# Kernel tuning notes

Measured on AMD Instinct MI355X. Metric: run time of the kernel, lower is better.

## Reference

```python
import jax, jax.numpy as jnp
import numpy as np

HIDDEN = 2048
N_HEADS = 32
N_KV_HEADS = 8
HEAD_DIM = HIDDEN // N_HEADS  # 64
N_GROUPS = N_HEADS // N_KV_HEADS  # 4
EPS = 1e-6
BATCH = 2
SEQ = 2048


def setup_inputs() -> dict:
    key = jax.random.key(0)
    ks = jax.random.split(key, 8)
    s = 1.0 / np.sqrt(HIDDEN)
    return {
        "hidden_states": jax.random.normal(ks[0], (BATCH, SEQ, HIDDEN), jnp.float32),
        # torch nn.Linear weights: [out_features, in_features]
        "Wq": jax.random.normal(ks[1], (N_HEADS * HEAD_DIM, HIDDEN), jnp.float32) * s,
        "Wk": jax.random.normal(ks[2], (N_KV_HEADS * HEAD_DIM, HIDDEN), jnp.float32) * s,
        "Wv": jax.random.normal(ks[3], (N_KV_HEADS * HEAD_DIM, HIDDEN), jnp.float32) * s,
        "Wo": jax.random.normal(ks[4], (HIDDEN, N_HEADS * HEAD_DIM), jnp.float32) * s,
        "q_norm_weight": jnp.ones((HEAD_DIM,), jnp.float32),
        "k_norm_weight": jnp.ones((HEAD_DIM,), jnp.float32),
    }


def _rmsnorm(x, w, eps=EPS):
    # x: [..., head_dim]
    rms = jax.lax.rsqrt(jnp.mean(x * x, axis=-1, keepdims=True) + eps)
    return x * rms * w


def reference(hidden_states, Wq, Wk, Wv, Wo, q_norm_weight, k_norm_weight):
    B, S, _ = hidden_states.shape
    # projections (y = x @ W.T)
    q = jnp.einsum('bsh,oh->bso', hidden_states, Wq)
    k = jnp.einsum('bsh,oh->bso', hidden_states, Wk)
    v = jnp.einsum('bsh,oh->bso', hidden_states, Wv)
    # [B, H, S, D]
    q = q.reshape(B, S, N_HEADS, HEAD_DIM).transpose(0, 2, 1, 3)
    k = k.reshape(B, S, N_KV_HEADS, HEAD_DIM).transpose(0, 2, 1, 3)
    v = v.reshape(B, S, N_KV_HEADS, HEAD_DIM).transpose(0, 2, 1, 3)
    # GQA repeat_interleave along head dim
    k = jnp.repeat(k, N_GROUPS, axis=1)
    v = jnp.repeat(v, N_GROUPS, axis=1)
    # fused QK RMSNorm
    q = _rmsnorm(q, q_norm_weight)
    k = _rmsnorm(k, k_norm_weight)
    # scaled dot-product attention with causal mask
    scale = 1.0 / np.sqrt(HEAD_DIM)
    scores = jnp.einsum('bhqd,bhkd->bhqk', q, k) * scale
    causal = jnp.tril(jnp.ones((S, S), dtype=bool))
    scores = jnp.where(causal, scores, jnp.finfo(scores.dtype).min)
    attn = jax.nn.softmax(scores, axis=-1)
    out = jnp.einsum('bhqk,bhkd->bhqd', attn, v)  # [B, H, S, D]
    out = out.transpose(0, 2, 1, 3).reshape(B, S, N_HEADS * HEAD_DIM)
    return jnp.einsum('bso,ho->bsh', out, Wo)
```

## Files before the change

### kernel.cpp

```cpp
#include <hip/hip_runtime.h>

typedef _Float16 f16;
typedef _Float16 f16x8 __attribute__((ext_vector_type(8)));
typedef _Float16 f16x4 __attribute__((ext_vector_type(4)));
typedef __fp16 fp16x2 __attribute__((ext_vector_type(2)));
typedef float f32x4 __attribute__((ext_vector_type(4)));

#define HID 2048
#define NH 32
#define NKV 8
#define HD 64
#define SEQ 2048
#define NB 2

__device__ __forceinline__ void gload_lds16(const void* g, void* l) {
  __builtin_amdgcn_global_load_lds((const __attribute__((address_space(1))) void*)g,
                                   (__attribute__((address_space(3))) void*)l, 16, 0, 0);
}

__device__ __forceinline__ uint cvt_pk_f16(float a, float b) {
  auto v = __builtin_amdgcn_cvt_pkrtz(a, b);
  uint u;
  __builtin_memcpy(&u, &v, 4);
  return u;
}

__device__ __forceinline__ float fdot2_ones(uint pk, float acc) {
  fp16x2 a;
  __builtin_memcpy(&a, &pk, 4);
  fp16x2 ones = {(__fp16)1.0f, (__fp16)1.0f};
  return __builtin_amdgcn_fdot2(a, ones, acc, false);
}

__device__ __forceinline__ float fast_exp2(float x) {
  float r;
  asm("v_exp_f32 %0, %1" : "=v"(r) : "v"(x));
  return r;
}

__global__ __launch_bounds__(256) void cvt_all(const float* __restrict__ X,
                                               const float* __restrict__ Wq,
                                               const float* __restrict__ Wk,
                                               const float* __restrict__ Wv,
                                               const float* __restrict__ Wo,
                                               f16* __restrict__ Xb, f16* __restrict__ Wqb,
                                               f16* __restrict__ Wkb, f16* __restrict__ Wvb,
                                               f16* __restrict__ Wob) {
  long i = (long)blockIdx.x * 256 + threadIdx.x;
  const float* s; f16* d; long o;
  if (i < 2097152)      { s = X;  d = Xb;  o = i; }
  else if (i < 3145728) { s = Wq; d = Wqb; o = i - 2097152; }
  else if (i < 3407872) { s = Wk; d = Wkb; o = i - 3145728; }
  else if (i < 3670016) { s = Wv; d = Wvb; o = i - 3407872; }
  else                  { s = Wo; d = Wob; o = i - 3670016; }
  float4 v = ((const float4*)s)[o];
  f16x4 ov = { (f16)v.x, (f16)v.y, (f16)v.z, (f16)v.w };
  ((f16x4*)d)[o] = ov;
}

__global__ __launch_bounds__(512, 2) void gemm256(const f16* __restrict__ A,
                                                  const f16* __restrict__ Bm,
                                                  f16* __restrict__ C0, f16* __restrict__ C1,
                                                  int M, int N, int K,
                                                  int n_split, int ldc0, int ldc1) {
  __shared__ f16 As[2][256 * 64];
  __shared__ f16 Bs[2][256 * 64];
  const int t = threadIdx.x, lane = t & 63, w = t >> 6;
  const int wr = w >> 2, wc = w & 3;
  const int g = lane >> 4, lr = lane & 15;

  const int nwg = gridDim.x * gridDim.y;
  const int orig = blockIdx.y * gridDim.x + blockIdx.x;
  const int wg = (orig & 7) * (nwg >> 3) + (orig >> 3);
  const int m0 = (wg / gridDim.x) * 256;
  const int n0 = (wg % gridDim.x) * 256;

  f32x4 acc[8][4] = {};
  const int nkt = K / 64;

  auto stage = [&](int buf, int kt) {
    const int k0 = kt * 64;
#pragma unroll
    for (int i = 0; i < 4; ++i) {
      int c = w * 4 + i;
      int o = c * 1024 + lane * 16;
      int row = o >> 7;
      int ss = ((o >> 4) & 7) ^ (row & 7);
      gload_lds16((const char*)A + ((size_t)(m0 + row) * K + k0) * 2 + ss * 16,
                  (char*)(&As[buf][0]) + c * 1024);
      gload_lds16((const char*)Bm + ((size_t)(n0 + row) * K + k0) * 2 + ss * 16,
                  (char*)(&Bs[buf][0]) + c * 1024);
    }
  };

  stage(0, 0);
  stage(1, 1);
  for (int kt = 0; kt < nkt; ++kt) {
    const int cur = kt & 1;
    if (kt + 1 < nkt) asm volatile("s_waitcnt vmcnt(8)" ::: "memory");
    else              asm volatile("s_waitcnt vmcnt(0)" ::: "memory");
    __builtin_amdgcn_s_barrier();
    __builtin_amdgcn_sched_barrier(0);

    const char* Ab = (const char*)(&As[cur][0]);
    const char* Bb = (const char*)(&Bs[cur][0]);
    f16x8 af[2][4], bf[2][4];

#pragma unroll
    for (int ks = 0; ks < 2; ++ks)
#pragma unroll
      for (int mf = 0; mf < 4; ++mf) {
        int row = wr * 128 + mf * 16 + lr;
        af[ks][mf] = *(const f16x8*)(Ab + row * 128 + (((g + 4 * ks) ^ (row & 7)) * 16));
      }
#pragma unroll
    for (int ks = 0; ks < 2; ++ks)
#pragma unroll
      for (int nf = 0; nf < 2; ++nf) {
        int row = wc * 64 + nf * 16 + lr;
        bf[ks][nf] = *(const f16x8*)(Bb + row * 128 + (((g + 4 * ks) ^ (row & 7)) * 16));
      }
    __builtin_amdgcn_s_setprio(1);
#pragma unroll
    for (int ks = 0; ks < 2; ++ks)
#pragma unroll
      for (int mf = 0; mf < 4; ++mf)
#pragma unroll
        for (int nf = 0; nf < 2; ++nf)
          acc[mf][nf] = __builtin_amdgcn_mfma_f32_16x16x32_f16(af[ks][mf], bf[ks][nf], acc[mf][nf], 0, 0, 0);
    __builtin_amdgcn_s_setprio(0);
    __builtin_amdgcn_sched_barrier(0);

#pragma unroll
    for (int ks = 0; ks < 2; ++ks)
#pragma unroll
      for (int nf = 2; nf < 4; ++nf) {
        int row = wc * 64 + nf * 16 + lr;
        bf[ks][nf] = *(const f16x8*)(Bb + row * 128 + (((g + 4 * ks) ^ (row & 7)) * 16));
      }
    __builtin_amdgcn_s_setprio(1);
#pragma unroll
    for (int ks = 0; ks < 2; ++ks)
#pragma unroll
      for (int mf = 0; mf < 4; ++mf)
#pragma unroll
        for (int nf = 2; nf < 4; ++nf)
          acc[mf][nf] = __builtin_amdgcn_mfma_f32_16x16x32_f16(af[ks][mf], bf[ks][nf], acc[mf][nf], 0, 0, 0);
    __builtin_amdgcn_s_setprio(0);
    __builtin_amdgcn_sched_barrier(0);

#pragma unroll
    for (int ks = 0; ks < 2; ++ks)
#pragma unroll
      for (int mf = 0; mf < 4; ++mf) {
        int row = wr * 128 + (mf + 4) * 16 + lr;
        af[ks][mf] = *(const f16x8*)(Ab + row * 128 + (((g + 4 * ks) ^ (row & 7)) * 16));
      }
    __builtin_amdgcn_s_setprio(1);
#pragma unroll
    for (int ks = 0; ks < 2; ++ks)
#pragma unroll
      for (int mf = 0; mf < 4; ++mf)
#pragma unroll
        for (int nf = 0; nf < 2; ++nf)
          acc[mf + 4][nf] = __builtin_amdgcn_mfma_f32_16x16x32_f16(af[ks][mf], bf[ks][nf], acc[mf + 4][nf], 0, 0, 0);
    __builtin_amdgcn_s_setprio(0);
    __builtin_amdgcn_sched_barrier(0);

    __builtin_amdgcn_s_setprio(1);
#pragma unroll
    for (int ks = 0; ks < 2; ++ks)
#pragma unroll
      for (int mf = 0; mf < 4; ++mf)
#pragma unroll
        for (int nf = 2; nf < 4; ++nf)
          acc[mf + 4][nf] = __builtin_amdgcn_mfma_f32_16x16x32_f16(af[ks][mf], bf[ks][nf], acc[mf + 4][nf], 0, 0, 0);
    __builtin_amdgcn_s_setprio(0);
    __builtin_amdgcn_sched_barrier(0);

    __builtin_amdgcn_s_barrier();
    __builtin_amdgcn_sched_barrier(0);
    if (kt + 2 < nkt) stage(cur, kt + 2);
  }

  f16* Cp; int ldc, nb;
  if (n0 < n_split) { Cp = C0; ldc = ldc0; nb = n0; }
  else              { Cp = C1; ldc = ldc1; nb = n0 - n_split; }
#pragma unroll
  for (int mf = 0; mf < 8; ++mf)
#pragma unroll
    for (int nf = 0; nf < 4; ++nf)
#pragma unroll
      for (int r = 0; r < 4; ++r) {
        int mm = m0 + wr * 128 + mf * 16 + g * 4 + r;
        int nn = nb + wc * 64 + nf * 16 + lr;
        Cp[(size_t)mm * ldc + nn] = (f16)acc[mf][nf][r];
      }
}

template <typename CT>
__global__ __launch_bounds__(256) void gemm_bt(const f16* __restrict__ A,
                                               const f16* __restrict__ Bm,
                                               CT* __restrict__ C0, CT* __restrict__ C1,
                                               int M, int N, int K,
                                               int n_split, int ldc0, int ldc1) {
  __shared__ f16 As[2][128 * 64];
  __shared__ f16 Bs[2][128 * 64];
  const int t = threadIdx.x;
  const int lane = t & 63;
  const int w = t >> 6;
  const int wr = w >> 1, wc = w & 1;
  const int g = lane >> 4;
  const int lr = lane & 15;

  const int nwg = gridDim.x * gridDim.y;
  const int orig = blockIdx.y * gridDim.x + blockIdx.x;
  const int wg = (orig & 7) * (nwg >> 3) + (orig >> 3);
  const int m0 = (wg / gridDim.x) * 128;
  const int n0 = (wg % gridDim.x) * 128;

  f32x4 acc[4][4] = {};

  const int nkt = K / 64;

  auto stage = [&](int buf, int kt) {
    const int k0 = kt * 64;
#pragma unroll
    for (int i = 0; i < 4; ++i) {
      int c = w * 4 + i;
      int o = c * 1024 + lane * 16;
      int row = o >> 7;
      int ss = ((o >> 4) & 7) ^ (row & 7);
      const char* srcA = (const char*)A + ((size_t)(m0 + row) * K + k0) * 2 + ss * 16;
      gload_lds16(srcA, (char*)(&As[buf][0]) + c * 1024);
      const char* srcB = (const char*)Bm + ((size_t)(n0 + row) * K + k0) * 2 + ss * 16;
      gload_lds16(srcB, (char*)(&Bs[buf][0]) + c * 1024);
    }
  };

  stage(0, 0);
  if (nkt > 1) stage(1, 1);
  for (int kt = 0; kt < nkt; ++kt) {
    const int cur = kt & 1;
    if (kt + 1 < nkt) asm volatile("s_waitcnt vmcnt(8)" ::: "memory");
    else              asm volatile("s_waitcnt vmcnt(0)" ::: "memory");
    __builtin_amdgcn_s_barrier();
    __builtin_amdgcn_sched_barrier(0);

    f16x8 af[2][4], bf[2][4];
#pragma unroll
    for (int ks = 0; ks < 2; ++ks)
#pragma unroll
      for (int mf = 0; mf < 4; ++mf) {
        int row = wr * 64 + mf * 16 + lr;
        int slot = (g + 4 * ks) ^ (row & 7);
        af[ks][mf] = *(const f16x8*)((const char*)(&As[cur][0]) + row * 128 + slot * 16);
      }
#pragma unroll
    for (int ks = 0; ks < 2; ++ks)
#pragma unroll
      for (int nf = 0; nf < 4; ++nf) {
        int row = wc * 64 + nf * 16 + lr;
        int slot = (g + 4 * ks) ^ (row & 7);
        bf[ks][nf] = *(const f16x8*)((const char*)(&Bs[cur][0]) + row * 128 + slot * 16);
      }
    asm volatile("s_waitcnt lgkmcnt(0)" ::: "memory");
    __builtin_amdgcn_sched_barrier(0);
    __builtin_amdgcn_s_barrier();

    if (kt + 2 < nkt) stage(cur, kt + 2);

    __builtin_amdgcn_s_setprio(1);
#pragma unroll
    for (int ks = 0; ks < 2; ++ks)
#pragma unroll
      for (int mf = 0; mf < 4; ++mf)
#pragma unroll
        for (int nf = 0; nf < 4; ++nf)
          acc[mf][nf] = __builtin_amdgcn_mfma_f32_16x16x32_f16(af[ks][mf], bf[ks][nf], acc[mf][nf], 0, 0, 0);
    __builtin_amdgcn_s_setprio(0);
  }

  CT* Cp; int ldc, nb;
  if (n0 < n_split) { Cp = C0; ldc = ldc0; nb = n0; }
  else              { Cp = C1; ldc = ldc1; nb = n0 - n_split; }
#pragma unroll
  for (int mf = 0; mf < 4; ++mf)
#pragma unroll
    for (int nf = 0; nf < 4; ++nf)
#pragma unroll
      for (int r = 0; r < 4; ++r) {
        int mm = m0 + wr * 64 + mf * 16 + g * 4 + r;
        int nn = nb + wc * 64 + nf * 16 + lr;
        Cp[(size_t)mm * ldc + nn] = (CT)acc[mf][nf][r];
      }
}

__global__ __launch_bounds__(256) void vtrans(f16* __restrict__ KV,
                                              f16* __restrict__ VT,
                                              const float* __restrict__ kw) {
  __shared__ f16 tile[64][72];
  int t = threadIdx.x;
  int st = blockIdx.x, hk = blockIdx.y, b = blockIdx.z;

#pragma unroll
  for (int p = 0; p < 2; ++p) {
    int idx = p * 256 + t;
    int s = idx >> 3, c8 = (idx & 7) * 8;
    f16* kp = KV + (size_t)(b * SEQ + st * 64 + s) * 1024 + hk * 64 + c8;
    f16x8 kv = *(const f16x8*)kp;
    float ss = 0.f;
#pragma unroll
    for (int j = 0; j < 8; ++j) { float x = (float)kv[j]; ss += x * x; }
    ss += __shfl_xor(ss, 1); ss += __shfl_xor(ss, 2); ss += __shfl_xor(ss, 4);
    float sc = rsqrtf(ss * (1.0f / 64.0f) + 1e-6f);
    f16x8 on;
#pragma unroll
    for (int j = 0; j < 8; ++j) on[j] = (f16)((float)kv[j] * sc * kw[c8 + j]);
    *(f16x8*)kp = on;
  }

#pragma unroll
  for (int p = 0; p < 2; ++p) {
    int idx = p * 256 + t;
    int s = idx >> 3, c8 = (idx & 7) * 8;
    f16x8 v = *(const f16x8*)(KV + (size_t)(b * SEQ + st * 64 + s) * 1024 + 512 + hk * 64 + c8);
    *(f16x8*)(&tile[s][c8]) = v;
  }
  __syncthreads();
#pragma unroll
  for (int p = 0; p < 2; ++p) {
    int idx = p * 256 + t;
    int d = idx >> 3, s8 = (idx & 7) * 8;
    f16x8 ov;
#pragma unroll
    for (int j = 0; j < 8; ++j) {
      int pos = s8 + j;
      int k = (pos & 32) | (((pos >> 2) & 1) << 4) | (((pos >> 4) & 1) << 3)
            | (((pos >> 3) & 1) << 2) | (pos & 3);
      ov[j] = tile[k][d];
    }
    *(f16x8*)(VT + ((size_t)((b * NKV + hk) * 64) + d) * SEQ + st * 64 + s8) = ov;
  }
}

__global__ __launch_bounds__(512) void attn(const f16* __restrict__ Q,
                                            const f16* __restrict__ KV,
                                            const f16* __restrict__ VT,
                                            f16* __restrict__ AO,
                                            const float* __restrict__ qw) {
  __shared__ f16 Ks[3][64 * 64];
  __shared__ f16 Vs[3][64 * 64];
  const int t = threadIdx.x, lane = t & 63, w = t >> 6;
  const int g = lane >> 4, lr = lane & 15;
  const int col = blockIdx.x;
  const int qt = 31 - blockIdx.y;
  const int b = col & 1;
  const int h = 2 * (col >> 1) + (w >> 2);
  const int rg = w & 3;
  const int hk = h >> 2;
  const int q0 = qt * 64;

  const size_t qrow = (size_t)(b * SEQ + q0 + rg * 16 + lr);
  f16x8 qf[2];
  qf[0] = *(const f16x8*)(Q + qrow * HID + h * 64 + g * 8);
  qf[1] = *(const f16x8*)(Q + qrow * HID + h * 64 + g * 8 + 32);

  {
    float ss = 0.f;
#pragma unroll
    for (int i = 0; i < 2; ++i)
#pragma unroll
      for (int j = 0; j < 8; ++j) { float x = (float)qf[i][j]; ss += x * x; }
    ss += __shfl_xor(ss, 16); ss += __shfl_xor(ss, 32);
    float sc = rsqrtf(ss * (1.0f / 64.0f) + 1e-6f) * (0.125f * 1.44269504f);
    const float4* qw4 = (const float4*)qw;
    float4 w0 = qw4[2 * g], w1 = qw4[2 * g + 1];
    float4 w2 = qw4[2 * g + 8], w3 = qw4[2 * g + 9];
    qf[0][0] = (f16)((float)qf[0][0] * sc * w0.x);
    qf[0][1] = (f16)((float)qf[0][1] * sc * w0.y);
    qf[0][2] = (f16)((float)qf[0][2] * sc * w0.z);
    qf[0][3] = (f16)((float)qf[0][3] * sc * w0.w);
    qf[0][4] = (f16)((float)qf[0][4] * sc * w1.x);
    qf[0][5] = (f16)((float)qf[0][5] * sc * w1.y);
    qf[0][6] = (f16)((float)qf[0][6] * sc * w1.z);
    qf[0][7] = (f16)((float)qf[0][7] * sc * w1.w);
    qf[1][0] = (f16)((float)qf[1][0] * sc * w2.x);
    qf[1][1] = (f16)((float)qf[1][1] * sc * w2.y);
    qf[1][2] = (f16)((float)qf[1][2] * sc * w2.z);
    qf[1][3] = (f16)((float)qf[1][3] * sc * w2.w);
    qf[1][4] = (f16)((float)qf[1][4] * sc * w3.x);
    qf[1][5] = (f16)((float)qf[1][5] * sc * w3.y);
    qf[1][6] = (f16)((float)qf[1][6] * sc * w3.z);
    qf[1][7] = (f16)((float)qf[1][7] * sc * w3.w);
  }

  int koff[2][4], voff[2][4];
#pragma unroll
  for (int ks = 0; ks < 2; ++ks)
#pragma unroll
    for (int nf = 0; nf < 4; ++nf) {
      int row = nf * 16 + lr;
      koff[ks][nf] = row * 128 + (((g + 4 * ks) ^ (row & 7)) * 16);
    }
#pragma unroll
  for (int m = 0; m < 2; ++m)
#pragma unroll
    for (int df = 0; df < 4; ++df) {
      int row = df * 16 + lr;
      voff[m][df] = row * 128 + (((4 * m + g) ^ (row & 7)) * 16);
    }

  f32x4 oacc[4] = {};
  float psum0 = 0.0f, psum1 = 0.0f;

  const int nkt = qt + 1;

  auto stage = [&](int buf, int kt2) {
    int o = w * 1024 + lane * 16;
    int row = o >> 7;
    int ss = ((o >> 4) & 7) ^ (row & 7);
    gload_lds16((const char*)KV + ((size_t)(b * SEQ + kt2 * 64 + row) * 1024 + hk * 64) * 2 + ss * 16,
                (char*)(&Ks[buf][0]) + w * 1024);
    gload_lds16((const char*)VT + (((size_t)((b * NKV + hk) * 64) + row) * SEQ + kt2 * 64) * 2 + ss * 16,
                (char*)(&Vs[buf][0]) + w * 1024);
  };

  stage(0, 0);
  if (nkt > 1) stage(1, 1);
  int cur = 0;
  for (int kt = 0; kt < nkt; ++kt) {
    if (kt + 1 < nkt) asm volatile("s_waitcnt vmcnt(2)" ::: "memory");
    else              asm volatile("s_waitcnt vmcnt(0)" ::: "memory");
    __builtin_amdgcn_s_barrier();
    asm volatile("" ::: "memory");

    if (kt + 2 < nkt) {
      int nb = cur + 2; if (nb >= 3) nb -= 3;
      stage(nb, kt + 2);
    }

    const char* Kb = (const char*)(&Ks[cur][0]);
    const char* Vb = (const char*)(&Vs[cur][0]);

    f32x4 sacc[4] = {};
#pragma unroll
    for (int ks = 0; ks < 2; ++ks) {
      __builtin_amdgcn_s_setprio(1);
#pragma unroll
      for (int nf = 0; nf < 4; ++nf) {
        f16x8 kf = *(const f16x8*)(Kb + koff[ks][nf]);
        sacc[nf] = __builtin_amdgcn_mfma_f32_16x16x32_f16(kf, qf[ks], sacc[nf], 0, 0, 0);
      }
      __builtin_amdgcn_s_setprio(0);
    }

    if (kt == qt) {
      int qq = q0 + rg * 16 + lr;
#pragma unroll
      for (int nf = 0; nf < 4; ++nf) {
        int kvb = kt * 64 + nf * 16 + g * 4;
#pragma unroll
        for (int r = 0; r < 4; ++r)
          if (kvb + r > qq) sacc[nf][r] = -1e30f;
      }
    }

    uint pk[8];
#pragma unroll
    for (int nf = 0; nf < 4; ++nf) {
      float p0 = fast_exp2(sacc[nf][0]);
      float p1 = fast_exp2(sacc[nf][1]);
      float p2 = fast_exp2(sacc[nf][2]);
      float p3 = fast_exp2(sacc[nf][3]);
      pk[2 * nf]     = cvt_pk_f16(p0, p1);
      pk[2 * nf + 1] = cvt_pk_f16(p2, p3);
      psum0 = fdot2_ones(pk[2 * nf], psum0);
      psum1 = fdot2_ones(pk[2 * nf + 1], psum1);
    }

#pragma unroll
    for (int m = 0; m < 2; ++m) {
      union { uint u[4]; f16x8 v; } pu;
      pu.u[0] = pk[4 * m];     pu.u[1] = pk[4 * m + 1];
      pu.u[2] = pk[4 * m + 2]; pu.u[3] = pk[4 * m + 3];
      __builtin_amdgcn_s_setprio(1);
#pragma unroll
      for (int df = 0; df < 4; ++df) {
        f16x8 vf = *(const f16x8*)(Vb + voff[m][df]);
        oacc[df] = __builtin_amdgcn_mfma_f32_16x16x32_f16(pu.v, vf, oacc[df], 0, 0, 0);
      }
      __builtin_amdgcn_s_setprio(0);
    }

    cur = (cur == 2) ? 0 : cur + 1;
  }

  float psum = psum0 + psum1;
  psum += __shfl_xor(psum, 16);
  psum += __shfl_xor(psum, 32);
  float pdiv[4];
#pragma unroll
  for (int r = 0; r < 4; ++r) pdiv[r] = 1.0f / __shfl(psum, g * 4 + r);

#pragma unroll
  for (int df = 0; df < 4; ++df)
#pragma unroll
    for (int r = 0; r < 4; ++r) {
      size_t rowg = (size_t)(b * SEQ + q0 + rg * 16 + g * 4 + r);
      AO[rowg * HID + h * 64 + df * 16 + lr] = (f16)(oacc[df][r] * pdiv[r]);
    }
}

extern "C" void kernel_launch(void* const* d_in, const int* in_sizes, int n_in,
                              void* d_out, int out_size, void* d_ws, size_t ws_size,
                              hipStream_t stream) {
  const float* X  = (const float*)d_in[0];
  const float* Wq = (const float*)d_in[1];
  const float* Wk = (const float*)d_in[2];
  const float* Wv = (const float*)d_in[3];
  const float* Wo = (const float*)d_in[4];
  const float* qw = (const float*)d_in[5];
  const float* kw = (const float*)d_in[6];

  char* ws = (char*)d_ws;
  f16* Xb   = (f16*)(ws + 0);
  f16* Wqkv = (f16*)(ws + 16777216);
  f16* Wob  = (f16*)(ws + 29360128);
  f16* Qb   = (f16*)(ws + 37748736);
  f16* KVb  = (f16*)(ws + 54525952);
  f16* VTb  = (f16*)(ws + 62914560);
  f16* AOb  = (f16*)(ws + 67108864);
  float* OUT = (float*)d_out;

  cvt_all<<<18432, 256, 0, stream>>>(X, Wq, Wk, Wv, Wo,
                                     Xb, Wqkv, Wqkv + 2048 * 2048, Wqkv + 2560 * 2048, Wob);

  gemm256<<<dim3(12, 16), 512, 0, stream>>>(Xb, Wqkv, Qb, KVb,
                                            4096, 3072, 2048, 2048, 2048, 1024);

  vtrans<<<dim3(32, 8, 2), 256, 0, stream>>>(KVb, VTb, kw);
  attn<<<dim3(32, 32, 1), 512, 0, stream>>>(Qb, KVb, VTb, AOb, qw);

  gemm_bt<float><<<dim3(16, 32), 256, 0, stream>>>(AOb, Wob, OUT, OUT,
                                                   4096, 2048, 2048, 2048, 2048, 2048);
}
```

Before: 169.0 us.

## Restructure QKV GEMM into 8-phase pipeline with half-tile staged loads

```diff
diff --git a/kernel.cpp b/kernel.cpp
--- a/kernel.cpp
+++ b/kernel.cpp
@@ -58,13 +58,13 @@
   ((f16x4*)d)[o] = ov;
 }
 
-__global__ __launch_bounds__(512, 2) void gemm256(const f16* __restrict__ A,
-                                                  const f16* __restrict__ Bm,
-                                                  f16* __restrict__ C0, f16* __restrict__ C1,
-                                                  int M, int N, int K,
-                                                  int n_split, int ldc0, int ldc1) {
-  __shared__ f16 As[2][256 * 64];
-  __shared__ f16 Bs[2][256 * 64];
+__global__ __launch_bounds__(512, 2) void gemm256_8p(const f16* __restrict__ A,
+                                                     const f16* __restrict__ Bm,
+                                                     f16* __restrict__ C0, f16* __restrict__ C1,
+                                                     int M, int N, int K,
+                                                     int n_split, int ldc0, int ldc1) {
+  __shared__ f16 Ah[2][2][128 * 64];
+  __shared__ f16 Bh[2][2][128 * 64];
   const int t = threadIdx.x, lane = t & 63, w = t >> 6;
   const int wr = w >> 2, wc = w & 3;
   const int g = lane >> 4, lr = lane & 15;
@@ -78,48 +78,71 @@
   f32x4 acc[8][4] = {};
   const int nkt = K / 64;
 
-  auto stage = [&](int buf, int kt) {
-    const int k0 = kt * 64;
-#pragma unroll
-    for (int i = 0; i < 4; ++i) {
-      int c = w * 4 + i;
-      int o = c * 1024 + lane * 16;
+  auto stageA = [&](int buf, int mh, int kt) {
+#pragma unroll
+    for (int c = 0; c < 2; ++c) {
+      int o = c * 8192 + w * 1024 + lane * 16;
       int row = o >> 7;
       int ss = ((o >> 4) & 7) ^ (row & 7);
-      gload_lds16((const char*)A + ((size_t)(m0 + row) * K + k0) * 2 + ss * 16,
-                  (char*)(&As[buf][0]) + c * 1024);
-      gload_lds16((const char*)Bm + ((size_t)(n0 + row) * K + k0) * 2 + ss * 16,
-                  (char*)(&Bs[buf][0]) + c * 1024);
+      gload_lds16((const char*)A + ((size_t)(m0 + mh * 128 + row) * K + kt * 64) * 2 + ss * 16,
+                  (char*)(&Ah[buf][mh][0]) + c * 8192 + w * 1024);
     }
   };
-
-  stage(0, 0);
-  stage(1, 1);
+  auto stageB = [&](int buf, int nh, int kt) {
+#pragma unroll
+    for (int c = 0; c < 2; ++c) {
+      int o = c * 8192 + w * 1024 + lane * 16;
+      int row = o >> 7;
+      int ss = ((o >> 4) & 7) ^ (row & 7);
+      gload_lds16((const char*)Bm + ((size_t)(n0 + nh * 128 + row) * K + kt * 64) * 2 + ss * 16,
+                  (char*)(&Bh[buf][nh][0]) + c * 8192 + w * 1024);
+    }
+  };
+
+  int aoff[2][8], boff[2][4];
+#pragma unroll
+  for (int ks = 0; ks < 2; ++ks) {
+#pragma unroll
+    for (int mf = 0; mf < 8; ++mf) {
+      int row = mf * 16 + lr;
+      aoff[ks][mf] = row * 128 + (((g + 4 * ks) ^ (row & 7)) * 16);
+    }
+#pragma unroll
+    for (int nf = 0; nf < 4; ++nf) {
+      int row = (wc & 1) * 64 + nf * 16 + lr;
+      boff[ks][nf] = row * 128 + (((g + 4 * ks) ^ (row & 7)) * 16);
+    }
+  }
+  const char* Abase[2] = { (const char*)(&Ah[0][wr][0]), (const char*)(&Ah[1][wr][0]) };
+  const char* Bbase[2] = { (const char*)(&Bh[0][wc >> 1][0]), (const char*)(&Bh[1][wc >> 1][0]) };
+
+  stageB(0, 0, 0); stageB(0, 1, 0);
+  stageA(0, 0, 0); stageA(0, 1, 0);
+  if (nkt > 1) {
+    stageB(1, 0, 1); stageB(1, 1, 1);
+    asm volatile("s_waitcnt vmcnt(4)" ::: "memory");
+  } else {
+    asm volatile("s_waitcnt vmcnt(0)" ::: "memory");
+  }
+  __builtin_amdgcn_s_barrier();
+
   for (int kt = 0; kt < nkt; ++kt) {
-    const int cur = kt & 1;
-    if (kt + 1 < nkt) asm volatile("s_waitcnt vmcnt(8)" ::: "memory");
-    else              asm volatile("s_waitcnt vmcnt(0)" ::: "memory");
-    __builtin_amdgcn_s_barrier();
-    __builtin_amdgcn_sched_barrier(0);
-
-    const char* Ab = (const char*)(&As[cur][0]);
-    const char* Bb = (const char*)(&Bs[cur][0]);
-    f16x8 af[2][4], bf[2][4];
-
-#pragma unroll
-    for (int ks = 0; ks < 2; ++ks)
-#pragma unroll
-      for (int mf = 0; mf < 4; ++mf) {
-        int row = wr * 128 + mf * 16 + lr;
-        af[ks][mf] = *(const f16x8*)(Ab + row * 128 + (((g + 4 * ks) ^ (row & 7)) * 16));
-      }
-#pragma unroll
-    for (int ks = 0; ks < 2; ++ks)
-#pragma unroll
-      for (int nf = 0; nf < 2; ++nf) {
-        int row = wc * 64 + nf * 16 + lr;
-        bf[ks][nf] = *(const f16x8*)(Bb + row * 128 + (((g + 4 * ks) ^ (row & 7)) * 16));
-      }
+    const int buf = kt & 1;
+    const char* Ab = Abase[buf];
+    const char* Bb = Bbase[buf];
+    f16x8 af[2][4], bf[2][2], bf2[2][2];
+
+#pragma unroll
+    for (int ks = 0; ks < 2; ++ks) {
+#pragma unroll
+      for (int mf = 0; mf < 4; ++mf) af[ks][mf] = *(const f16x8*)(Ab + aoff[ks][mf]);
+#pragma unroll
+      for (int nf = 0; nf < 2; ++nf) bf[ks][nf] = *(const f16x8*)(Bb + boff[ks][nf]);
+    }
+    if (kt + 1 < nkt) stageA(buf ^ 1, 0, kt + 1);
+    asm volatile("s_waitcnt lgkmcnt(8)" ::: "memory");
+    __builtin_amdgcn_s_barrier();
+    asm volatile("s_waitcnt lgkmcnt(0)" ::: "memory");
     __builtin_amdgcn_s_setprio(1);
 #pragma unroll
     for (int ks = 0; ks < 2; ++ks)
@@ -129,33 +152,33 @@
         for (int nf = 0; nf < 2; ++nf)
           acc[mf][nf] = __builtin_amdgcn_mfma_f32_16x16x32_f16(af[ks][mf], bf[ks][nf], acc[mf][nf], 0, 0, 0);
     __builtin_amdgcn_s_setprio(0);
-    __builtin_amdgcn_sched_barrier(0);
-
-#pragma unroll
-    for (int ks = 0; ks < 2; ++ks)
-#pragma unroll
-      for (int nf = 2; nf < 4; ++nf) {
-        int row = wc * 64 + nf * 16 + lr;
-        bf[ks][nf] = *(const f16x8*)(Bb + row * 128 + (((g + 4 * ks) ^ (row & 7)) * 16));
-      }
+    __builtin_amdgcn_s_barrier();
+
+#pragma unroll
+    for (int ks = 0; ks < 2; ++ks)
+#pragma unroll
+      for (int nf = 0; nf < 2; ++nf) bf2[ks][nf] = *(const f16x8*)(Bb + boff[ks][nf + 2]);
+    if (kt + 1 < nkt) stageA(buf ^ 1, 1, kt + 1);
+    __builtin_amdgcn_s_barrier();
+    asm volatile("s_waitcnt lgkmcnt(0)" ::: "memory");
     __builtin_amdgcn_s_setprio(1);
 #pragma unroll
     for (int ks = 0; ks < 2; ++ks)
 #pragma unroll
       for (int mf = 0; mf < 4; ++mf)
 #pragma unroll
-        for (int nf = 2; nf < 4; ++nf)
-          acc[mf][nf] = __builtin_amdgcn_mfma_f32_16x16x32_f16(af[ks][mf], bf[ks][nf], acc[mf][nf], 0, 0, 0);
+        for (int nf = 0; nf < 2; ++nf)
+          acc[mf][nf + 2] = __builtin_amdgcn_mfma_f32_16x16x32_f16(af[ks][mf], bf2[ks][nf], acc[mf][nf + 2], 0, 0, 0);
     __builtin_amdgcn_s_setprio(0);
-    __builtin_amdgcn_sched_barrier(0);
-
-#pragma unroll
-    for (int ks = 0; ks < 2; ++ks)
-#pragma unroll
-      for (int mf = 0; mf < 4; ++mf) {
-        int row = wr * 128 + (mf + 4) * 16 + lr;
-        af[ks][mf] = *(const f16x8*)(Ab + row * 128 + (((g + 4 * ks) ^ (row & 7)) * 16));
-      }
+    __builtin_amdgcn_s_barrier();
+
+#pragma unroll
+    for (int ks = 0; ks < 2; ++ks)
+#pragma unroll
+      for (int mf = 0; mf < 4; ++mf) af[ks][mf] = *(const f16x8*)(Ab + aoff[ks][mf + 4]);
+    if (kt + 2 < nkt) stageB(buf, 0, kt + 2);
+    __builtin_amdgcn_s_barrier();
+    asm volatile("s_waitcnt lgkmcnt(0)" ::: "memory");
     __builtin_amdgcn_s_setprio(1);
 #pragma unroll
     for (int ks = 0; ks < 2; ++ks)
@@ -165,22 +188,25 @@
         for (int nf = 0; nf < 2; ++nf)
           acc[mf + 4][nf] = __builtin_amdgcn_mfma_f32_16x16x32_f16(af[ks][mf], bf[ks][nf], acc[mf + 4][nf], 0, 0, 0);
     __builtin_amdgcn_s_setprio(0);
-    __builtin_amdgcn_sched_barrier(0);
-
+    __builtin_amdgcn_s_barrier();
+
+    if (kt + 2 < nkt) {
+      stageB(buf, 1, kt + 2);
+      asm volatile("s_waitcnt vmcnt(4)" ::: "memory");
+    } else {
+      asm volatile("s_waitcnt vmcnt(0)" ::: "memory");
+    }
+    __builtin_amdgcn_s_barrier();
     __builtin_amdgcn_s_setprio(1);
 #pragma unroll
     for (int ks = 0; ks < 2; ++ks)
 #pragma unroll
       for (int mf = 0; mf < 4; ++mf)
 #pragma unroll
-        for (int nf = 2; nf < 4; ++nf)
-          acc[mf + 4][nf] = __builtin_amdgcn_mfma_f32_16x16x32_f16(af[ks][mf], bf[ks][nf], acc[mf + 4][nf], 0, 0, 0);
+        for (int nf = 0; nf < 2; ++nf)
+          acc[mf + 4][nf + 2] = __builtin_amdgcn_mfma_f32_16x16x32_f16(af[ks][mf], bf2[ks][nf], acc[mf + 4][nf + 2], 0, 0, 0);
     __builtin_amdgcn_s_setprio(0);
-    __builtin_amdgcn_sched_barrier(0);
-
-    __builtin_amdgcn_s_barrier();
-    __builtin_amdgcn_sched_barrier(0);
-    if (kt + 2 < nkt) stage(cur, kt + 2);
+    __builtin_amdgcn_s_barrier();
   }
 
   f16* Cp; int ldc, nb;
@@ -536,8 +562,8 @@
   cvt_all<<<18432, 256, 0, stream>>>(X, Wq, Wk, Wv, Wo,
                                      Xb, Wqkv, Wqkv + 2048 * 2048, Wqkv + 2560 * 2048, Wob);
 
-  gemm256<<<dim3(12, 16), 512, 0, stream>>>(Xb, Wqkv, Qb, KVb,
-                                            4096, 3072, 2048, 2048, 2048, 1024);
+  gemm256_8p<<<dim3(12, 16), 512, 0, stream>>>(Xb, Wqkv, Qb, KVb,
+                                               4096, 3072, 2048, 2048, 2048, 1024);
 
   vtrans<<<dim3(32, 8, 2), 256, 0, stream>>>(KVb, VTb, kw);
   attn<<<dim3(32, 32, 1), 512, 0, stream>>>(Qb, KVb, VTb, AOb, qw);
```

Result: slower. 217.2 us (+28.5%).
